# Kernel optimization log

Measured on AMD Instinct MI355X. Metric: run time of the kernel, lower is better.

## Reference

```python
import jax, jax.numpy as jnp
import numpy as np

V, E, B, NODES_PER_GRAPH = 100000, 128, 4096, 64
N = B * NODES_PER_GRAPH  # 262144 nodes per side
EPS = 1e-6


def setup_inputs() -> dict:
    key = jax.random.key(0)
    k1, k2, k3, k4, k5, k6 = jax.random.split(key, 6)
    left_x = jax.random.randint(k1, (N, 1), 0, V, dtype=jnp.int64 if jax.config.jax_enable_x64 else jnp.int32)
    right_x = jax.random.randint(k2, (N, 1), 0, V, dtype=left_x.dtype)
    # sorted segment ids with every graph non-empty (64 nodes per graph)
    batch_ids = jnp.repeat(jnp.arange(B, dtype=left_x.dtype), NODES_PER_GRAPH)
    label = jax.random.randint(k3, (B,), 0, 2).astype(jnp.float32)
    emb_table = jax.random.normal(k4, (V, E), dtype=jnp.float32)
    W = jax.random.normal(k5, (E, E), dtype=jnp.float32) / np.sqrt(E)
    b = jax.random.normal(k6, (E,), dtype=jnp.float32) * 0.01
    return {
        "left_x": left_x,
        "left_graph_index": jnp.arange(B, dtype=left_x.dtype),
        "right_x": right_x,
        "right_graph_index": jnp.arange(B, dtype=left_x.dtype),
        "left_x_batch": batch_ids,
        "right_x_batch": batch_ids,
        "label": label,
        "emb_table": emb_table,
        "W": W,
        "b": b,
    }


def _side_emb(x, x_batch, emb_table, W, b, num_segments):
    node_emb = emb_table[x[:, 0]]                       # [N, E] gather
    pooled = jax.ops.segment_max(node_emb, x_batch,      # [B, E] scatter-max
                                 num_segments=num_segments,
                                 indices_are_sorted=True)
    return pooled @ W.T + b                              # trans_linear


def reference(left_x, left_graph_index, right_x, right_graph_index,
              left_x_batch, right_x_batch, label, emb_table, W, b):
    num_segments = label.shape[0]
    left_final = _side_emb(left_x, left_x_batch, emb_table, W, b, num_segments)
    right_final = _side_emb(right_x, right_x_batch, emb_table, W, b, num_segments)
    # torch CosineSimilarity(eps=1e-6): clamp each norm at eps
    dot = jnp.sum(left_final * right_final, axis=-1)
    nl = jnp.maximum(jnp.linalg.norm(left_final, axis=-1), EPS)
    nr = jnp.maximum(jnp.linalg.norm(right_final, axis=-1), EPS)
    cos = dot / (nl * nr)                                # [B]
    # ContrastiveLoss(margin=1.0), size_average=True
    losses = 0.5 * ((1.0 - label) * cos ** 2
                    + label * jnp.maximum(1.0 - cos, 0.0) ** 2)
    sim_loss = losses.mean()
    return sim_loss, cos
```

## Files before the change

### kernel.cpp

```cpp
#include <hip/hip_runtime.h>
#include <math.h>

#define B_GRAPHS 4096
#define NPG 64
#define E_DIM 128
#define GPG 16

__global__ __launch_bounds__(256) void gather_max_k(
    const int* __restrict__ lx, const int* __restrict__ rx,
    const float* __restrict__ emb, float* __restrict__ pooled)
{
    const int g    = blockIdx.x;
    const int side = blockIdx.y;
    const int* __restrict__ x = side ? rx : lx;
    const int t = threadIdx.x;

    __shared__ int idx[NPG];
    if (t < NPG) idx[t] = x[g * NPG + t];
    __syncthreads();

    const int n0 = t >> 5;
    const int q  = t & 31;

    float4 acc = make_float4(-INFINITY, -INFINITY, -INFINITY, -INFINITY);
    #pragma unroll
    for (int i = 0; i < 8; ++i) {
        const int n = (i << 3) + n0;
        const float4* __restrict__ row =
            reinterpret_cast<const float4*>(emb + (size_t)idx[n] * E_DIM);
        const float4 v = row[q];
        acc.x = fmaxf(acc.x, v.x);
        acc.y = fmaxf(acc.y, v.y);
        acc.z = fmaxf(acc.z, v.z);
        acc.w = fmaxf(acc.w, v.w);
    }

    __shared__ float4 red[256];
    red[t] = acc;
    __syncthreads();
    if (t < 32) {
        float4 m = red[t];
        #pragma unroll
        for (int j = 1; j < 8; ++j) {
            const float4 v = red[j * 32 + t];
            m.x = fmaxf(m.x, v.x);
            m.y = fmaxf(m.y, v.y);
            m.z = fmaxf(m.z, v.z);
            m.w = fmaxf(m.w, v.w);
        }
        float4* __restrict__ dst = reinterpret_cast<float4*>(
            pooled + ((size_t)side * B_GRAPHS + g) * E_DIM);
        dst[t] = m;
    }
}

__global__ __launch_bounds__(256) void matvec_cos_k(
    const float* __restrict__ pooled, const float* __restrict__ W,
    const float* __restrict__ bias, const float* __restrict__ label,
    float* __restrict__ cos_out, float* __restrict__ partial)
{
    __shared__ float Wl[E_DIM * (E_DIM + 1)];
    __shared__ float P[2][E_DIM];
    __shared__ float F[2][E_DIM];

    const int t = threadIdx.x;
    for (int i = t; i < E_DIM * E_DIM; i += 256)
        Wl[(i >> 7) * (E_DIM + 1) + (i & 127)] = W[i];

    const int side = t >> 7;
    const int e    = t & 127;
    const float be = bias[e];
    float lossAcc = 0.0f;
    __syncthreads();

    for (int gi = 0; gi < GPG; ++gi) {
        const int g = blockIdx.x * GPG + gi;
        P[side][e] = pooled[((size_t)side * B_GRAPHS + g) * E_DIM + e];
        __syncthreads();

        float acc = be;
        const float* __restrict__ wr = &Wl[e * (E_DIM + 1)];
        const float* __restrict__ pv = P[side];
        #pragma unroll 8
        for (int f = 0; f < E_DIM; ++f)
            acc = fmaf(pv[f], wr[f], acc);
        F[side][e] = acc;
        __syncthreads();

        if (t < 64) {
            const float l0 = F[0][t], l1 = F[0][t + 64];
            const float r0 = F[1][t], r1 = F[1][t + 64];
            float dot = l0 * r0 + l1 * r1;
            float nl  = l0 * l0 + l1 * l1;
            float nr  = r0 * r0 + r1 * r1;
            #pragma unroll
            for (int off = 32; off; off >>= 1) {
                dot += __shfl_down(dot, off, 64);
                nl  += __shfl_down(nl,  off, 64);
                nr  += __shfl_down(nr,  off, 64);
            }
            if (t == 0) {
                const float nlv = fmaxf(sqrtf(nl), 1e-6f);
                const float nrv = fmaxf(sqrtf(nr), 1e-6f);
                const float c   = dot / (nlv * nrv);
                cos_out[g] = c;
                const float lab = label[g];
                const float mm  = fmaxf(1.0f - c, 0.0f);
                lossAcc += 0.5f * ((1.0f - lab) * c * c + lab * mm * mm);
            }
        }
        __syncthreads();
    }
    if (t == 0) partial[blockIdx.x] = lossAcc;
}

__global__ void loss_reduce_k(const float* __restrict__ partial,
                              float* __restrict__ out, int n)
{
    const int t = threadIdx.x;
    float s = 0.0f;
    for (int i = t; i < n; i += 64) s += partial[i];
    #pragma unroll
    for (int off = 32; off; off >>= 1) s += __shfl_down(s, off, 64);
    if (t == 0) out[0] = s * (1.0f / (float)B_GRAPHS);
}

extern "C" void kernel_launch(void* const* d_in, const int* in_sizes, int n_in,
                              void* d_out, int out_size, void* d_ws, size_t ws_size,
                              hipStream_t stream)
{
    const int*   lx    = (const int*)d_in[0];
    const int*   rx    = (const int*)d_in[2];
    const float* label = (const float*)d_in[6];
    const float* emb   = (const float*)d_in[7];
    const float* W     = (const float*)d_in[8];
    const float* bias  = (const float*)d_in[9];

    float* out     = (float*)d_out;
    float* pooled  = (float*)d_ws;
    float* partial = pooled + (size_t)2 * B_GRAPHS * E_DIM;

    dim3 g1(B_GRAPHS, 2);
    gather_max_k<<<g1, 256, 0, stream>>>(lx, rx, emb, pooled);

    matvec_cos_k<<<B_GRAPHS / GPG, 256, 0, stream>>>(
        pooled, W, bias, label, out + 1, partial);

    loss_reduce_k<<<1, 64, 0, stream>>>(partial, out, B_GRAPHS / GPG);
}
```

Before: 169.0 us.

## Fuse gather-max, linear, cosine and loss into one per-graph kernel

Merges the three kernels into a single kernel with one block per graph. Each block gathers both sides, pools them, computes the linear layer by reading W straight from global memory (L2-cached) instead of staging it in LDS, then computes the cosine and atomically adds its scaled loss into the output. This drops the pooled round trip through memory and two launches. In exchange, 4096 atomics contend on one address, a memset is added, and the summation order becomes nondeterministic.

```diff
diff --git a/kernel.cpp b/kernel.cpp
--- a/kernel.cpp
+++ b/kernel.cpp
@@ -4,125 +4,104 @@
 #define B_GRAPHS 4096
 #define NPG 64
 #define E_DIM 128
-#define GPG 16
+#define INV_B (1.0f / 4096.0f)
 
-__global__ __launch_bounds__(256) void gather_max_k(
+__global__ __launch_bounds__(256) void fused_graph_sim_k(
     const int* __restrict__ lx, const int* __restrict__ rx,
-    const float* __restrict__ emb, float* __restrict__ pooled)
+    const float* __restrict__ emb, const float* __restrict__ W,
+    const float* __restrict__ bias, const float* __restrict__ label,
+    float* __restrict__ out)
 {
-    const int g    = blockIdx.x;
-    const int side = blockIdx.y;
-    const int* __restrict__ x = side ? rx : lx;
+    const int g = blockIdx.x;
     const int t = threadIdx.x;
 
-    __shared__ int idx[NPG];
-    if (t < NPG) idx[t] = x[g * NPG + t];
+    __shared__ int   idxL[NPG], idxR[NPG];
+    __shared__ float4 redL[256], redR[256];
+    __shared__ float4 P4[2][32];
+    __shared__ float  F[2][E_DIM];
+
+    if (t < NPG)            idxL[t]        = lx[g * NPG + t];
+    else if (t < 2 * NPG)   idxR[t - NPG]  = rx[g * NPG + (t - NPG)];
     __syncthreads();
 
     const int n0 = t >> 5;
     const int q  = t & 31;
-
-    float4 acc = make_float4(-INFINITY, -INFINITY, -INFINITY, -INFINITY);
+    float4 aL = make_float4(-INFINITY, -INFINITY, -INFINITY, -INFINITY);
+    float4 aR = aL;
     #pragma unroll
     for (int i = 0; i < 8; ++i) {
         const int n = (i << 3) + n0;
-        const float4* __restrict__ row =
-            reinterpret_cast<const float4*>(emb + (size_t)idx[n] * E_DIM);
-        const float4 v = row[q];
-        acc.x = fmaxf(acc.x, v.x);
-        acc.y = fmaxf(acc.y, v.y);
-        acc.z = fmaxf(acc.z, v.z);
-        acc.w = fmaxf(acc.w, v.w);
+        const float4 vL =
+            reinterpret_cast<const float4*>(emb + (size_t)idxL[n] * E_DIM)[q];
+        const float4 vR =
+            reinterpret_cast<const float4*>(emb + (size_t)idxR[n] * E_DIM)[q];
+        aL.x = fmaxf(aL.x, vL.x); aL.y = fmaxf(aL.y, vL.y);
+        aL.z = fmaxf(aL.z, vL.z); aL.w = fmaxf(aL.w, vL.w);
+        aR.x = fmaxf(aR.x, vR.x); aR.y = fmaxf(aR.y, vR.y);
+        aR.z = fmaxf(aR.z, vR.z); aR.w = fmaxf(aR.w, vR.w);
     }
+    redL[t] = aL;
+    redR[t] = aR;
+    __syncthreads();
 
-    __shared__ float4 red[256];
-    red[t] = acc;
-    __syncthreads();
-    if (t < 32) {
-        float4 m = red[t];
+    if (t < 64) {
+        const int side = t >> 5;
+        const int qq   = t & 31;
+        const float4* __restrict__ src = side ? redR : redL;
+        float4 m = src[qq];
         #pragma unroll
         for (int j = 1; j < 8; ++j) {
-            const float4 v = red[j * 32 + t];
-            m.x = fmaxf(m.x, v.x);
-            m.y = fmaxf(m.y, v.y);
-            m.z = fmaxf(m.z, v.z);
-            m.w = fmaxf(m.w, v.w);
+            const float4 v = src[j * 32 + qq];
+            m.x = fmaxf(m.x, v.x); m.y = fmaxf(m.y, v.y);
+            m.z = fmaxf(m.z, v.z); m.w = fmaxf(m.w, v.w);
         }
-        float4* __restrict__ dst = reinterpret_cast<float4*>(
-            pooled + ((size_t)side * B_GRAPHS + g) * E_DIM);
-        dst[t] = m;
+        P4[side][qq] = m;
     }
-}
-
-__global__ __launch_bounds__(256) void matvec_cos_k(
-    const float* __restrict__ pooled, const float* __restrict__ W,
-    const float* __restrict__ bias, const float* __restrict__ label,
-    float* __restrict__ cos_out, float* __restrict__ partial)
-{
-    __shared__ float Wl[E_DIM * (E_DIM + 1)];
-    __shared__ float P[2][E_DIM];
-    __shared__ float F[2][E_DIM];
-
-    const int t = threadIdx.x;
-    for (int i = t; i < E_DIM * E_DIM; i += 256)
-        Wl[(i >> 7) * (E_DIM + 1) + (i & 127)] = W[i];
-
-    const int side = t >> 7;
-    const int e    = t & 127;
-    const float be = bias[e];
-    float lossAcc = 0.0f;
     __syncthreads();
 
-    for (int gi = 0; gi < GPG; ++gi) {
-        const int g = blockIdx.x * GPG + gi;
-        P[side][e] = pooled[((size_t)side * B_GRAPHS + g) * E_DIM + e];
-        __syncthreads();
+    {
+        const int side = t & 1;
+        const int e    = t >> 1;
+        float acc = bias[e];
+        const float4* __restrict__ wr =
+            reinterpret_cast<const float4*>(W + (size_t)e * E_DIM);
+        const float4* __restrict__ pv = P4[side];
+        #pragma unroll 8
+        for (int fi = 0; fi < 32; ++fi) {
+            const float4 wv = wr[fi];
+            const float4 p  = pv[fi];
+            acc = fmaf(p.x, wv.x, acc);
+            acc = fmaf(p.y, wv.y, acc);
+            acc = fmaf(p.z, wv.z, acc);
+            acc = fmaf(p.w, wv.w, acc);
+        }
+        F[side][e] = acc;
+    }
+    __syncthreads();
 
-        float acc = be;
-        const float* __restrict__ wr = &Wl[e * (E_DIM + 1)];
-        const float* __restrict__ pv = P[side];
-        #pragma unroll 8
-        for (int f = 0; f < E_DIM; ++f)
-            acc = fmaf(pv[f], wr[f], acc);
-        F[side][e] = acc;
-        __syncthreads();
-
-        if (t < 64) {
-            const float l0 = F[0][t], l1 = F[0][t + 64];
-            const float r0 = F[1][t], r1 = F[1][t + 64];
-            float dot = l0 * r0 + l1 * r1;
-            float nl  = l0 * l0 + l1 * l1;
-            float nr  = r0 * r0 + r1 * r1;
-            #pragma unroll
-            for (int off = 32; off; off >>= 1) {
-                dot += __shfl_down(dot, off, 64);
-                nl  += __shfl_down(nl,  off, 64);
-                nr  += __shfl_down(nr,  off, 64);
-            }
-            if (t == 0) {
-                const float nlv = fmaxf(sqrtf(nl), 1e-6f);
-                const float nrv = fmaxf(sqrtf(nr), 1e-6f);
-                const float c   = dot / (nlv * nrv);
-                cos_out[g] = c;
-                const float lab = label[g];
-                const float mm  = fmaxf(1.0f - c, 0.0f);
-                lossAcc += 0.5f * ((1.0f - lab) * c * c + lab * mm * mm);
-            }
+    if (t < 64) {
+        const float l0 = F[0][t], l1 = F[0][t + 64];
+        const float r0 = F[1][t], r1 = F[1][t + 64];
+        float dot = l0 * r0 + l1 * r1;
+        float nl  = l0 * l0 + l1 * l1;
+        float nr  = r0 * r0 + r1 * r1;
+        #pragma unroll
+        for (int off = 32; off; off >>= 1) {
+            dot += __shfl_down(dot, off);
+            nl  += __shfl_down(nl,  off);
+            nr  += __shfl_down(nr,  off);
         }
-        __syncthreads();
+        if (t == 0) {
+            const float nlv = fmaxf(sqrtf(nl), 1e-6f);
+            const float nrv = fmaxf(sqrtf(nr), 1e-6f);
+            const float c   = dot / (nlv * nrv);
+            out[1 + g] = c;
+            const float lab = label[g];
+            const float mm  = fmaxf(1.0f - c, 0.0f);
+            const float loss = 0.5f * ((1.0f - lab) * c * c + lab * mm * mm);
+            atomicAdd(out, loss * INV_B);
+        }
     }
-    if (t == 0) partial[blockIdx.x] = lossAcc;
-}
-
-__global__ void loss_reduce_k(const float* __restrict__ partial,
-                              float* __restrict__ out, int n)
-{
-    const int t = threadIdx.x;
-    float s = 0.0f;
-    for (int i = t; i < n; i += 64) s += partial[i];
-    #pragma unroll
-    for (int off = 32; off; off >>= 1) s += __shfl_down(s, off, 64);
-    if (t == 0) out[0] = s * (1.0f / (float)B_GRAPHS);
 }
 
 extern "C" void kernel_launch(void* const* d_in, const int* in_sizes, int n_in,
@@ -136,15 +115,10 @@
     const float* W     = (const float*)d_in[8];
     const float* bias  = (const float*)d_in[9];
 
-    float* out     = (float*)d_out;
-    float* pooled  = (float*)d_ws;
-    float* partial = pooled + (size_t)2 * B_GRAPHS * E_DIM;
+    float* out = (float*)d_out;
 
-    dim3 g1(B_GRAPHS, 2);
-    gather_max_k<<<g1, 256, 0, stream>>>(lx, rx, emb, pooled);
+    hipMemsetAsync(out, 0, sizeof(float), stream);
 
-    matvec_cos_k<<<B_GRAPHS / GPG, 256, 0, stream>>>(
-        pooled, W, bias, label, out + 1, partial);
-
-    loss_reduce_k<<<1, 64, 0, stream>>>(partial, out, B_GRAPHS / GPG);
+    fused_graph_sim_k<<<B_GRAPHS, 256, 0, stream>>>(
+        lx, rx, emb, W, bias, label, out);
 }
```

Result: faster. 160.6 us (-4.9%).
